# Performance work log

Measured on AMD Instinct MI355X. Metric: run time of the kernel, lower is better.

The kernel has to match this reference:

```python
import jax, jax.numpy as jnp
import numpy as np

B, T, NCH, NBIN, NBAND = 2, 400, 8, 512, 40
NPV = NCH * NCH


def setup_inputs() -> dict:
    key = jax.random.key(0)
    ks = jax.random.split(key, 7)
    bins_real = jax.random.normal(ks[0], (B, T, NCH, NBIN), jnp.float32)
    bins_imag = jax.random.normal(ks[1], (B, T, NCH, NBIN), jnp.float32)
    band_matrix_real = jax.random.normal(ks[2], (NBIN, NBAND), jnp.float32) * 0.05
    band_matrix_imag = jax.random.normal(ks[3], (NBIN, NBAND), jnp.float32) * 0.05
    cov_to_pv_real = jax.random.normal(ks[4], (NPV, NCH * NCH), jnp.float32) * 0.1
    cov_to_pv_imag = jax.random.normal(ks[5], (NPV, NCH * NCH), jnp.float32) * 0.1
    tau = jax.random.uniform(ks[6], (NBAND,), jnp.float32, 0.8, 0.99)
    return {
        'bins_real': bins_real, 'bins_imag': bins_imag,
        'band_matrix_real': band_matrix_real, 'band_matrix_imag': band_matrix_imag,
        'cov_to_pv_real': cov_to_pv_real, 'cov_to_pv_imag': cov_to_pv_imag,
        'tau': tau,
    }


def _power_vector(bins_real, bins_imag, band_matrix_real, band_matrix_imag,
                  cov_to_pv_real, cov_to_pv_imag, tau):
    x = jax.lax.complex(bins_real, bins_imag)            # (B,T,C,F)
    nch = x.shape[-2]
    EPS = 1e-20
    # per-bin covariance outer product, flattened cov dim: (B,T,F,C*C)
    cov = jnp.einsum('btif,btjf->btfij', x, jnp.conj(x))
    b, t, f = cov.shape[:3]
    cov = cov.reshape(b, t, f, nch * nch)
    diag = jnp.arange(nch) * (nch + 1)                   # diagonal indices in cov dim
    trace = jnp.clip(jnp.sum(cov.real[..., diag], axis=-1, keepdims=True), EPS, None)
    cov = cov / trace                                    # per-bin trace normalisation
    # phase adjustment along the bin axis (n=1 -> lag of 2 bins)
    c = jnp.swapaxes(cov, -1, -2)                        # (B,T,C2,F)
    prod = jnp.conj(c[..., :-2]) * c[..., 2:]
    ang = jnp.arctan2(prod.imag, prod.real)
    ang = jnp.concatenate([ang[..., :1], ang, ang[..., -1:]], axis=-1)  # edge pad
    adj = jnp.abs(c) * jax.lax.complex(jnp.cos(ang), jnp.sin(ang))
    adj = adj.at[..., diag, :].set(c[..., diag, :])      # keep original diagonals
    # band projection: contract bins against (F,K) band matrix
    bm = jax.lax.complex(band_matrix_real, band_matrix_imag)
    band_cov = jnp.einsum('btcf,fk->btkc', adj, bm)      # (B,T,K,C2)
    dsum = jnp.clip(band_cov.real[..., diag].sum(-1, keepdims=True), EPS, None)
    band_cov = band_cov / dsum
    # first-order IIR smoothing over frames, per-band pole tau
    a = tau[:, None].astype(band_cov.real.dtype)         # (K,1)
    def step(carry, xt):
        y = a * carry + (1.0 - a) * xt
        return y, y
    y0 = jnp.zeros_like(band_cov[:, 0])                  # (B,K,C2)
    _, ys = jax.lax.scan(step, y0, jnp.moveaxis(band_cov, 1, 0))
    band_cov = jnp.moveaxis(ys, 0, 1)                    # (B,T,K,C2)
    # cov -> power vector projection, real part
    c2p = jax.lax.complex(cov_to_pv_real, cov_to_pv_imag)  # (P,C2)
    pv = jnp.einsum('pc,btkc->btkp', c2p, band_cov).real   # (B,T,K,P)
    return pv


def reference(bins_real, bins_imag, band_matrix_real, band_matrix_imag,
              cov_to_pv_real, cov_to_pv_imag, tau):
    return _power_vector(bins_real, bins_imag, band_matrix_real, band_matrix_imag,
                         cov_to_pv_real, cov_to_pv_imag, tau)
```

## Files before the change

kernel.cpp:

```cpp
#include <hip/hip_runtime.h>

#define B_    2
#define T_    400
#define NCH_  8
#define NBIN_ 512
#define NBAND_ 40
#define NPV_  64

using short8  = __attribute__((ext_vector_type(8))) short;
using float4v = __attribute__((ext_vector_type(4))) float;

static __device__ inline unsigned pkbf(float x, float y) {
  union { float f; unsigned u; } a, b;
  a.f = x; b.f = y;
  unsigned ra = a.u + 0x7fffu + ((a.u >> 16) & 1u);
  unsigned rb = b.u + 0x7fffu + ((b.u >> 16) & 1u);
  return (ra >> 16) | (rb & 0xffff0000u);
}
static __device__ inline void upk(unsigned u, float& lo, float& hi) {
  union { unsigned q; float f; } a, b;
  a.q = u << 16; b.q = u & 0xffff0000u;
  lo = a.f; hi = b.f;
}
static __device__ inline unsigned swapvar(unsigned u) {
  unsigned r = u ^ 0x80000000u;
  return (r >> 16) | (r << 16);
}

__global__ __launch_bounds__(256) void pv_prep(
    const float* __restrict__ bmr, const float* __restrict__ bmi,
    const float* __restrict__ c2pr, const float* __restrict__ c2pi,
    float* __restrict__ ws)
{
  const int tid = threadIdx.x;
  const int blk = blockIdx.x;
  if (blk == 0) {
    __shared__ float sds[256];
    int k = tid & 63, part = tid >> 6;
    float s = 0.f;
    if (k < NBAND_) {
      const float* col = bmr + k;
      #pragma unroll 16
      for (int f = part * 128; f < part * 128 + 128; f++) s += col[f * 40];
    }
    sds[tid] = s;
    __syncthreads();
    if (tid < NBAND_) {
      float t = sds[tid] + sds[tid + 64] + sds[tid + 128] + sds[tid + 192];
      ws[tid] = 1.0f / fmaxf(t, 1e-20f);
    }
  } else if (blk <= 24) {
    int F = (blk - 1) * 256 + tid;
    int l = F & 63;
    int fid = F >> 6;
    int s5 = fid / 3;
    int n = fid - s5 * 3;
    int k = n * 16 + (l & 15);
    int quad = l >> 4;
    unsigned dw[4];
    #pragma unroll
    for (int t2 = 0; t2 < 4; t2++) {
      float v0 = 0.f, v1 = 0.f;
      if (k < NBAND_) {
        int f = s5 * 16 + quad * 4 + t2;
        v0 = bmr[f * 40 + k]; v1 = bmi[f * 40 + k];
      }
      dw[t2] = pkbf(v0, v1);
    }
    ((uint4*)((char*)ws + 1024))[F] = make_uint4(dw[0], dw[1], dw[2], dw[3]);
  } else {
    int F2 = (blk - 25) * 256 + tid;
    int lane = F2 & 63, E = F2 >> 6;
    int nt = E >> 2, ks = E & 3;
    int n = lane & 15, quad = lane >> 4;
    int p = nt * 16 + n;
    unsigned dw[4];
    #pragma unroll
    for (int t2 = 0; t2 < 4; t2++) {
      int c = ks * 16 + quad * 4 + t2;
      dw[t2] = pkbf(c2pr[p * 64 + c], -c2pi[p * 64 + c]);
    }
    ((uint4*)((char*)ws + 197632))[E * 64 + lane] = make_uint4(dw[0], dw[1], dw[2], dw[3]);
  }
}

__global__ __launch_bounds__(256)
__attribute__((amdgpu_waves_per_eu(3, 4)))
void pv_main(
    const float* __restrict__ br, const float* __restrict__ bi,
    const float* __restrict__ ws, float* __restrict__ out)
{
  __shared__ __align__(16) unsigned smem[4176];
  unsigned* vsh  = smem;
  float*    dssh = (float*)(smem + 4128);

  const int bt  = blockIdx.x;
  const int tid = threadIdx.x;
  const float* pr  = br + (size_t)bt * (NCH_ * NBIN_);
  const float* pim = bi + (size_t)bt * (NCH_ * NBIN_);

  const int mt   = tid >> 6;
  const int lane = tid & 63;
  const int m16  = lane & 15;
  const int quad = lane >> 4;
  const int p    = mt * 16 + m16;
  const int ich  = p >> 3, jch = p & 7;
  const uint4* BFl = ((const uint4*)((const char*)ws + 1024)) + lane;

  uint4 BFp[4][3];
  #pragma unroll
  for (int d = 0; d < 4; d++)
    #pragma unroll
    for (int n = 0; n < 3; n++) BFp[d][n] = BFl[(d * 3 + n) * 64];

  #pragma unroll
  for (int fs = 0; fs < 2; fs++) {
    const int f = fs * 256 + tid;
    const int fm = (f == 0) ? 0 : ((f == 511) ? 509 : f - 1);
    const int fp = (f == 0) ? 2 : ((f == 511) ? 511 : f + 1);
    float tr = 0.f;
    float t1[8], t2[8];
    #pragma unroll
    for (int c = 0; c < 8; c++) {
      const float* cr = pr + c * 512;
      const float* ci = pim + c * 512;
      float xr = cr[f],   xi = ci[f];
      float xrm = cr[fm], xim = ci[fm];
      float xrp = cr[fp], xip = ci[fp];
      tr = fmaf(xr, xr, tr); tr = fmaf(xi, xi, tr);
      float Gr = fmaf(xrm, xrp,  xim * xip);
      float Gi = fmaf(xrm, xip, -(xim * xrp));
      float am = fmaxf(fmaxf(fabsf(Gr), fabsf(Gi)), 1e-30f);
      float rc = __builtin_amdgcn_rcpf(am);
      float q1 = Gr * rc, q2 = Gi * rc;
      float n2 = fmaf(q1, q1, q2 * q2);
      float rn = __builtin_amdgcn_rsqf(n2);
      bool ok = n2 > 0.f;
      float ur = ok ? q1 * rn : 1.f;
      float ui = ok ? q2 * rn : 0.f;
      float mg = __builtin_amdgcn_sqrtf(fmaf(xr, xr, xi * xi));
      t1[c] = mg * ur; t2[c] = mg * ui;
    }
    float scv = __builtin_amdgcn_rsqf(fmaxf(tr, 1e-20f));
    #pragma unroll
    for (int c = 0; c < 8; c++)
      vsh[c * 516 + f] = pkbf(t1[c] * scv, t2[c] * scv);
  }
  __syncthreads();

  const uint4* Avp = (const uint4*)(vsh + ich * 516) + quad;
  const uint4* Bvp = (const uint4*)(vsh + jch * 516) + quad;

  float4v acc[6];
  #pragma unroll
  for (int g = 0; g < 6; g++) acc[g] = (float4v){0.f, 0.f, 0.f, 0.f};

  uint4 Apre[2], Bpre[2];
  Apre[0] = Avp[0]; Bpre[0] = Bvp[0];
  Apre[1] = Avp[4]; Bpre[1] = Bvp[4];

  #pragma unroll
  for (int s = 0; s < 32; s++) {
    const int c2 = s & 1;
    const int c4 = s & 3;
    uint4 av = Apre[c2], bv = Bpre[c2];
    uint4 cb[3];
    #pragma unroll
    for (int n = 0; n < 3; n++) cb[n] = BFp[c4][n];
    if (s + 2 < 32) {
      Apre[c2] = Avp[(s + 2) * 4];
      Bpre[c2] = Bvp[(s + 2) * 4];
    }
    if (s + 4 < 32) {
      #pragma unroll
      for (int n = 0; n < 3; n++) BFp[c4][n] = BFl[((s + 4) * 3 + n) * 64];
    }
    float ar[4], ai[4];
    {
      float vr, vi, wr, wi;
      upk(av.x, vr, vi); upk(bv.x, wr, wi);
      ar[0] = fmaf(vr, wr,  vi * wi); ai[0] = fmaf(vi, wr, -(vr * wi));
      upk(av.y, vr, vi); upk(bv.y, wr, wi);
      ar[1] = fmaf(vr, wr,  vi * wi); ai[1] = fmaf(vi, wr, -(vr * wi));
      upk(av.z, vr, vi); upk(bv.z, wr, wi);
      ar[2] = fmaf(vr, wr,  vi * wi); ai[2] = fmaf(vi, wr, -(vr * wi));
      upk(av.w, vr, vi); upk(bv.w, wr, wi);
      ar[3] = fmaf(vr, wr,  vi * wi); ai[3] = fmaf(vi, wr, -(vr * wi));
    }
    uint4 au1 = make_uint4(pkbf(ar[0], -ai[0]), pkbf(ar[1], -ai[1]),
                           pkbf(ar[2], -ai[2]), pkbf(ar[3], -ai[3]));
    uint4 au2 = make_uint4(swapvar(au1.x), swapvar(au1.y),
                           swapvar(au1.z), swapvar(au1.w));
    short8 af1 = __builtin_bit_cast(short8, au1);
    short8 af2 = __builtin_bit_cast(short8, au2);
    #pragma unroll
    for (int n = 0; n < 3; n++) {
      short8 bfrag = __builtin_bit_cast(short8, cb[n]);
      acc[n]     = __builtin_amdgcn_mfma_f32_16x16x32_bf16(af1, bfrag, acc[n],     0, 0, 0);
      acc[n + 3] = __builtin_amdgcn_mfma_f32_16x16x32_bf16(af2, bfrag, acc[n + 3], 0, 0, 0);
    }
  }

  const uint4* EF = ((const uint4*)((const char*)ws + 197632)) + (mt * 4) * 64 + lane;
  uint4 eb[4];
  #pragma unroll
  for (int ks = 0; ks < 4; ks++) eb[ks] = EF[ks * 64];
  if (tid < 48) dssh[tid] = (tid < NBAND_) ? ws[tid] : 0.f;

  __syncthreads();
  unsigned* bcsh = smem;
  #pragma unroll
  for (int n = 0; n < 3; n++) {
    uint4 w4 = make_uint4(pkbf(acc[n][0], acc[n + 3][0]),
                          pkbf(acc[n][1], acc[n + 3][1]),
                          pkbf(acc[n][2], acc[n + 3][2]),
                          pkbf(acc[n][3], acc[n + 3][3]));
    *(uint4*)(bcsh + (n * 16 + m16) * 68 + mt * 16 + quad * 4) = w4;
  }
  __syncthreads();

  float4v eacc[3];
  #pragma unroll
  for (int kt = 0; kt < 3; kt++) eacc[kt] = (float4v){0.f, 0.f, 0.f, 0.f};
  #pragma unroll
  for (int ks = 0; ks < 4; ks++) {
    short8 bfr = __builtin_bit_cast(short8, eb[ks]);
    #pragma unroll
    for (int kt = 0; kt < 3; kt++) {
      uint4 a4 = *(const uint4*)(bcsh + (kt * 16 + m16) * 68 + ks * 16 + quad * 4);
      short8 afr = __builtin_bit_cast(short8, a4);
      eacc[kt] = __builtin_amdgcn_mfma_f32_16x16x32_bf16(afr, bfr, eacc[kt], 0, 0, 0);
    }
  }
  float* op = out + (size_t)bt * (NBAND_ * NPV_);
  #pragma unroll
  for (int kt = 0; kt < 3; kt++) {
    #pragma unroll
    for (int r = 0; r < 4; r++) {
      int k = kt * 16 + quad * 4 + r;
      if (k < NBAND_)
        op[k * 64 + mt * 16 + m16] = eacc[kt][r] * dssh[k];
    }
  }
}

__global__ __launch_bounds__(256) void pv_iir3(float* __restrict__ z,
                                               const float* __restrict__ tau)
{
  __shared__ float gsh[16][16];
  const int pg = blockIdx.x & 3;
  const int bk = blockIdx.x >> 2;
  const int k = bk % NBAND_;
  const int b = bk / NBAND_;
  const float a  = tau[k];
  const float om = 1.0f - a;
  const int c  = threadIdx.x >> 4;
  const int pl = threadIdx.x & 15;
  const int p  = pg * 16 + pl;
  const size_t stride = (size_t)NBAND_ * 64;
  size_t idx0 = (size_t)b * (T_ * NBAND_ * 64) + (size_t)(c * 25) * stride + k * 64 + p;

  float y[25];
  float accv = 0.f;
  #pragma unroll
  for (int i = 0; i < 25; i++) {
    float v = z[idx0 + (size_t)i * stride];
    accv = fmaf(a, accv, om * v);
    y[i] = accv;
  }
  gsh[c][pl] = accv;
  __syncthreads();
  float a2 = a * a, a8 = a2 * a2 * a2 * a2, a16 = a8 * a8;
  float A = a16 * a8 * a;
  float H = 0.f;
  #pragma unroll
  for (int d = 0; d < 15; d++) {
    if (d < c) H = fmaf(A, H, gsh[d][pl]);
  }
  float wp = a;
  #pragma unroll
  for (int i = 0; i < 25; i++) {
    z[idx0 + (size_t)i * stride] = fmaf(wp, H, y[i]);
    wp *= a;
  }
}

extern "C" void kernel_launch(void* const* d_in, const int* in_sizes, int n_in,
                              void* d_out, int out_size, void* d_ws, size_t ws_size,
                              hipStream_t stream)
{
  const float* br   = (const float*)d_in[0];
  const float* bi   = (const float*)d_in[1];
  const float* bmr  = (const float*)d_in[2];
  const float* bmi  = (const float*)d_in[3];
  const float* c2pr = (const float*)d_in[4];
  const float* c2pi = (const float*)d_in[5];
  const float* tau  = (const float*)d_in[6];
  float* out = (float*)d_out;
  float* ws  = (float*)d_ws;

  hipLaunchKernelGGL(pv_prep, dim3(29), dim3(256), 0, stream,
                     bmr, bmi, c2pr, c2pi, ws);
  hipLaunchKernelGGL(pv_main, dim3(B_ * T_), dim3(256), 0, stream,
                     br, bi, ws, out);
  hipLaunchKernelGGL(pv_iir3, dim3(B_ * NBAND_ * 4), dim3(256), 0, stream,
                     out, tau);
}
```

Baseline: 117.7 us.

## Stage band-matrix MFMA fragments through double-buffered LDS via direct global-to-LDS loads

Instead of each thread prefetching band-matrix B-fragments from global memory into registers, each block now copies them cooperatively into a double-buffered LDS region using global_load_lds, with a barrier per stage of four k-steps. The aim is to cut register pressure and redundant per-wave global traffic. The LDS row padding for the per-bin vectors is removed (516 to 512), the diagonal-sum scale is read straight from global memory instead of LDS, and launch bounds change from a waves-per-EU hint to a min-blocks hint. The trade-offs are much larger LDS use (about 40KB per block), which can lower occupancy, eight extra barriers, and possible LDS bank conflicts now that the padding is gone.

```diff
diff --git a/kernel.cpp b/kernel.cpp
--- a/kernel.cpp
+++ b/kernel.cpp
@@ -25,6 +25,13 @@
 static __device__ inline unsigned swapvar(unsigned u) {
   unsigned r = u ^ 0x80000000u;
   return (r >> 16) | (r << 16);
+}
+static __device__ inline void gld_lds16(const uint4* g, uint4* l) {
+  auto* lds_ptr = reinterpret_cast<__attribute__((address_space(3))) uint4*>(
+      reinterpret_cast<uintptr_t>(l));
+  auto* g_ptr = reinterpret_cast<const __attribute__((address_space(1))) uint4*>(
+      reinterpret_cast<uintptr_t>(g));
+  __builtin_amdgcn_global_load_lds(g_ptr, lds_ptr, 16, 0, 0);
 }
 
 __global__ __launch_bounds__(256) void pv_prep(
@@ -84,15 +91,13 @@
   }
 }
 
-__global__ __launch_bounds__(256)
-__attribute__((amdgpu_waves_per_eu(3, 4)))
-void pv_main(
+__global__ __launch_bounds__(256, 4) void pv_main(
     const float* __restrict__ br, const float* __restrict__ bi,
     const float* __restrict__ ws, float* __restrict__ out)
 {
-  __shared__ __align__(16) unsigned smem[4176];
-  unsigned* vsh  = smem;
-  float*    dssh = (float*)(smem + 4128);
+  __shared__ __align__(16) unsigned smem[10240];
+  unsigned* vsh = smem;
+  uint4*    bst = (uint4*)(smem + 4096);
 
   const int bt  = blockIdx.x;
   const int tid = threadIdx.x;
@@ -105,13 +110,15 @@
   const int quad = lane >> 4;
   const int p    = mt * 16 + m16;
   const int ich  = p >> 3, jch = p & 7;
-  const uint4* BFl = ((const uint4*)((const char*)ws + 1024)) + lane;
-
-  uint4 BFp[4][3];
-  #pragma unroll
-  for (int d = 0; d < 4; d++)
-    #pragma unroll
-    for (int n = 0; n < 3; n++) BFp[d][n] = BFl[(d * 3 + n) * 64];
+  const uint4* BF0 = (const uint4*)((const char*)ws + 1024);
+
+  {
+    const uint4* g = BF0 + tid;
+    uint4* l = bst + tid;
+    gld_lds16(g, l);
+    gld_lds16(g + 256, l + 256);
+    gld_lds16(g + 512, l + 512);
+  }
 
   #pragma unroll
   for (int fs = 0; fs < 2; fs++) {
@@ -144,70 +151,70 @@
     float scv = __builtin_amdgcn_rsqf(fmaxf(tr, 1e-20f));
     #pragma unroll
     for (int c = 0; c < 8; c++)
-      vsh[c * 516 + f] = pkbf(t1[c] * scv, t2[c] * scv);
+      vsh[c * 512 + f] = pkbf(t1[c] * scv, t2[c] * scv);
   }
   __syncthreads();
 
-  const uint4* Avp = (const uint4*)(vsh + ich * 516) + quad;
-  const uint4* Bvp = (const uint4*)(vsh + jch * 516) + quad;
+  const uint4* Avp = (const uint4*)(vsh + ich * 512) + quad;
+  const uint4* Bvp = (const uint4*)(vsh + jch * 512) + quad;
 
   float4v acc[6];
   #pragma unroll
   for (int g = 0; g < 6; g++) acc[g] = (float4v){0.f, 0.f, 0.f, 0.f};
 
-  uint4 Apre[2], Bpre[2];
-  Apre[0] = Avp[0]; Bpre[0] = Bvp[0];
-  Apre[1] = Avp[4]; Bpre[1] = Bvp[4];
-
-  #pragma unroll
-  for (int s = 0; s < 32; s++) {
-    const int c2 = s & 1;
-    const int c4 = s & 3;
-    uint4 av = Apre[c2], bv = Bpre[c2];
-    uint4 cb[3];
-    #pragma unroll
-    for (int n = 0; n < 3; n++) cb[n] = BFp[c4][n];
-    if (s + 2 < 32) {
-      Apre[c2] = Avp[(s + 2) * 4];
-      Bpre[c2] = Bvp[(s + 2) * 4];
-    }
-    if (s + 4 < 32) {
-      #pragma unroll
-      for (int n = 0; n < 3; n++) BFp[c4][n] = BFl[((s + 4) * 3 + n) * 64];
-    }
-    float ar[4], ai[4];
-    {
-      float vr, vi, wr, wi;
-      upk(av.x, vr, vi); upk(bv.x, wr, wi);
-      ar[0] = fmaf(vr, wr,  vi * wi); ai[0] = fmaf(vi, wr, -(vr * wi));
-      upk(av.y, vr, vi); upk(bv.y, wr, wi);
-      ar[1] = fmaf(vr, wr,  vi * wi); ai[1] = fmaf(vi, wr, -(vr * wi));
-      upk(av.z, vr, vi); upk(bv.z, wr, wi);
-      ar[2] = fmaf(vr, wr,  vi * wi); ai[2] = fmaf(vi, wr, -(vr * wi));
-      upk(av.w, vr, vi); upk(bv.w, wr, wi);
-      ar[3] = fmaf(vr, wr,  vi * wi); ai[3] = fmaf(vi, wr, -(vr * wi));
-    }
-    uint4 au1 = make_uint4(pkbf(ar[0], -ai[0]), pkbf(ar[1], -ai[1]),
-                           pkbf(ar[2], -ai[2]), pkbf(ar[3], -ai[3]));
-    uint4 au2 = make_uint4(swapvar(au1.x), swapvar(au1.y),
-                           swapvar(au1.z), swapvar(au1.w));
-    short8 af1 = __builtin_bit_cast(short8, au1);
-    short8 af2 = __builtin_bit_cast(short8, au2);
-    #pragma unroll
-    for (int n = 0; n < 3; n++) {
-      short8 bfrag = __builtin_bit_cast(short8, cb[n]);
-      acc[n]     = __builtin_amdgcn_mfma_f32_16x16x32_bf16(af1, bfrag, acc[n],     0, 0, 0);
-      acc[n + 3] = __builtin_amdgcn_mfma_f32_16x16x32_bf16(af2, bfrag, acc[n + 3], 0, 0, 0);
-    }
+  for (int st = 0; st < 8; st++) {
+    if (st < 7) {
+      const uint4* g = BF0 + (st + 1) * 768 + tid;
+      uint4* l = bst + ((st + 1) & 1) * 768 + tid;
+      gld_lds16(g, l);
+      gld_lds16(g + 256, l + 256);
+      gld_lds16(g + 512, l + 512);
+    }
+    const uint4* bb = bst + (st & 1) * 768;
+    #pragma unroll
+    for (int q = 0; q < 4; q++) {
+      const int s = st * 4 + q;
+      uint4 av = Avp[s * 4];
+      uint4 bv = Bvp[s * 4];
+      uint4 cb0 = bb[(q * 3 + 0) * 64 + lane];
+      uint4 cb1 = bb[(q * 3 + 1) * 64 + lane];
+      uint4 cb2 = bb[(q * 3 + 2) * 64 + lane];
+      float ar[4], ai[4];
+      {
+        float vr, vi, wr, wi;
+        upk(av.x, vr, vi); upk(bv.x, wr, wi);
+        ar[0] = fmaf(vr, wr,  vi * wi); ai[0] = fmaf(vi, wr, -(vr * wi));
+        upk(av.y, vr, vi); upk(bv.y, wr, wi);
+        ar[1] = fmaf(vr, wr,  vi * wi); ai[1] = fmaf(vi, wr, -(vr * wi));
+        upk(av.z, vr, vi); upk(bv.z, wr, wi);
+        ar[2] = fmaf(vr, wr,  vi * wi); ai[2] = fmaf(vi, wr, -(vr * wi));
+        upk(av.w, vr, vi); upk(bv.w, wr, wi);
+        ar[3] = fmaf(vr, wr,  vi * wi); ai[3] = fmaf(vi, wr, -(vr * wi));
+      }
+      uint4 au1 = make_uint4(pkbf(ar[0], -ai[0]), pkbf(ar[1], -ai[1]),
+                             pkbf(ar[2], -ai[2]), pkbf(ar[3], -ai[3]));
+      uint4 au2 = make_uint4(swapvar(au1.x), swapvar(au1.y),
+                             swapvar(au1.z), swapvar(au1.w));
+      short8 af1 = __builtin_bit_cast(short8, au1);
+      short8 af2 = __builtin_bit_cast(short8, au2);
+      short8 b0 = __builtin_bit_cast(short8, cb0);
+      short8 b1 = __builtin_bit_cast(short8, cb1);
+      short8 b2 = __builtin_bit_cast(short8, cb2);
+      acc[0] = __builtin_amdgcn_mfma_f32_16x16x32_bf16(af1, b0, acc[0], 0, 0, 0);
+      acc[3] = __builtin_amdgcn_mfma_f32_16x16x32_bf16(af2, b0, acc[3], 0, 0, 0);
+      acc[1] = __builtin_amdgcn_mfma_f32_16x16x32_bf16(af1, b1, acc[1], 0, 0, 0);
+      acc[4] = __builtin_amdgcn_mfma_f32_16x16x32_bf16(af2, b1, acc[4], 0, 0, 0);
+      acc[2] = __builtin_amdgcn_mfma_f32_16x16x32_bf16(af1, b2, acc[2], 0, 0, 0);
+      acc[5] = __builtin_amdgcn_mfma_f32_16x16x32_bf16(af2, b2, acc[5], 0, 0, 0);
+    }
+    __syncthreads();
   }
 
   const uint4* EF = ((const uint4*)((const char*)ws + 197632)) + (mt * 4) * 64 + lane;
   uint4 eb[4];
   #pragma unroll
   for (int ks = 0; ks < 4; ks++) eb[ks] = EF[ks * 64];
-  if (tid < 48) dssh[tid] = (tid < NBAND_) ? ws[tid] : 0.f;
-
-  __syncthreads();
+
   unsigned* bcsh = smem;
   #pragma unroll
   for (int n = 0; n < 3; n++) {
@@ -233,13 +240,16 @@
     }
   }
   float* op = out + (size_t)bt * (NBAND_ * NPV_);
+  const float4* wsd = (const float4*)ws;
   #pragma unroll
   for (int kt = 0; kt < 3; kt++) {
+    float4 dv = wsd[kt * 4 + quad];
+    float dva[4] = {dv.x, dv.y, dv.z, dv.w};
     #pragma unroll
     for (int r = 0; r < 4; r++) {
       int k = kt * 16 + quad * 4 + r;
       if (k < NBAND_)
-        op[k * 64 + mt * 16 + m16] = eacc[kt][r] * dssh[k];
+        op[k * 64 + mt * 16 + m16] = eacc[kt][r] * dva[r];
     }
   }
 }
```

After: 119.8 us. Within noise of the previous version (+1.8%).
